# Performance work log

Measured on AMD Instinct MI355X. Metric: run time of the kernel, lower is better.

The kernel has to match this reference:

```python
import jax, jax.numpy as jnp
import numpy as np

FIX_SCALE = np.array([[0.,0.,0.],[1.,0.,0.],[0.,1.,0.],[0.,0.,1.],[-1.,0.,0.],[0.,-1.,0.]], dtype=np.float32)
NUM_HEADS = 8
ATTN_DIMS = 512
HEAD_DIMS = ATTN_DIMS // NUM_HEADS
NUM_LEARN = 6
SIG_CLAMP = 9.21  # safe_sigmoid clamp


def quat_to_rotmat(q):
    # q: [G,4] (w,x,y,z), normalized -> [G,3,3]
    q = q / jnp.linalg.norm(q, axis=-1, keepdims=True)
    w, x, y, z = q[..., 0], q[..., 1], q[..., 2], q[..., 3]
    r0 = jnp.stack([1 - 2*(y*y + z*z), 2*(x*y - w*z), 2*(x*z + w*y)], -1)
    r1 = jnp.stack([2*(x*y + w*z), 1 - 2*(x*x + z*z), 2*(y*z - w*x)], -1)
    r2 = jnp.stack([2*(x*z - w*y), 2*(y*z + w*x), 1 - 2*(x*x + y*y)], -1)
    return jnp.stack([r0, r1, r2], -2)


def bilinear_sample(fm, gx, gy):
    # fm: [C,H,W]; gx,gy: [...] in [-1,1]; align_corners=False, zero padding
    C, H, W = fm.shape
    x = (gx + 1.0) * (W * 0.5) - 0.5
    y = (gy + 1.0) * (H * 0.5) - 0.5
    x0 = jnp.floor(x); y0 = jnp.floor(y)
    wx1 = x - x0; wx0 = 1.0 - wx1
    wy1 = y - y0; wy0 = 1.0 - wy1

    def gather(xf, yf):
        xi = xf.astype(jnp.int32); yi = yf.astype(jnp.int32)
        valid = (xi >= 0) & (xi < W) & (yi >= 0) & (yi < H)
        xi = jnp.clip(xi, 0, W - 1); yi = jnp.clip(yi, 0, H - 1)
        return fm[:, yi, xi] * valid[None].astype(fm.dtype)  # [C, ...]

    out = (gather(x0, y0) * (wx0 * wy0)[None]
           + gather(x0 + 1, y0) * (wx1 * wy0)[None]
           + gather(x0, y0 + 1) * (wx0 * wy1)[None]
           + gather(x0 + 1, y0 + 1) * (wx1 * wy1)[None])
    return jnp.moveaxis(out, 0, -1)  # [..., C]


def setup_inputs() -> dict:
    key = jax.random.key(0)
    ks = jax.random.split(key, 16)
    G, BS, GFD = 8192, 1, 32
    means = jax.random.uniform(ks[0], (G, 3), minval=-1.0, maxval=1.0)
    means = means.at[:, 2].add(3.0)  # push in front of camera
    scales = jax.random.uniform(ks[1], (G, 3), minval=0.01, maxval=0.1)
    rotations = jax.random.normal(ks[2], (G, 4))
    features = jax.random.normal(ks[3], (BS, G, 3, GFD))
    transforms = jnp.tile(jnp.eye(4)[None], (G, 1, 1)) + 0.01 * jax.random.normal(ks[4], (G, 4, 4))
    f = 64.0
    proj = jnp.array([[f, 0., 32., 0.], [0., f, 32., 0.], [0., 0., 1., 0.], [0., 0., 0., 1.]], dtype=jnp.float32)
    projection = jnp.tile(proj[None], (BS, 1, 1))
    image_features = jax.random.normal(ks[5], (BS, 256, 64, 64))
    s = lambda d: 1.0 / np.sqrt(d)
    Wq = jax.random.normal(ks[6], (GFD, ATTN_DIMS)) * s(GFD)
    Wk = jax.random.normal(ks[7], (ATTN_DIMS, 256)) * s(256)
    Wv = jax.random.normal(ks[8], (ATTN_DIMS, 256)) * s(256)
    W_off = jax.random.normal(ks[9], (HEAD_DIMS + 3, NUM_LEARN * 3)) * s(HEAD_DIMS + 3)
    b_off = jnp.zeros((NUM_LEARN * 3,))
    Wout = jax.random.normal(ks[10], (ATTN_DIMS, GFD)) * s(ATTN_DIMS)
    b_out = jnp.zeros((GFD,))
    return {"means": means, "scales": scales, "rotations": rotations, "features": features,
            "transforms": transforms, "projection": projection, "image_features": image_features,
            "Wq": Wq, "Wk": Wk, "Wv": Wv, "W_off": W_off, "b_off": b_off, "Wout": Wout, "b_out": b_out}


def reference(means, scales, rotations, features, transforms, projection, image_features,
              Wq, Wk, Wv, W_off, b_off, Wout, b_out):
    G = means.shape[0]
    bs = features.shape[0]
    H, HD = NUM_HEADS, HEAD_DIMS
    h_img, w_img = image_features.shape[-2:]

    # queries: [bs,G,3,attn] -> [bs,H,G,3,hd]
    q_full = jnp.einsum('bgtf,fa->bgta', features, Wq)
    q = q_full.reshape(bs, G, 3, H, HD).transpose(0, 3, 1, 2, 4)

    # transform means to world space with per-gaussian 4x4
    homo = jnp.concatenate([means, jnp.ones((G, 1), means.dtype)], -1)  # [G,4]
    means_w = jnp.einsum('gij,gj->gi', transforms, homo)[:, :3]  # [G,3]

    # OffsetNet: per-head learnable offsets from (world mean, token-mean query)
    q_mean = q.mean(axis=3)  # [bs,H,G,hd]
    m_b = jnp.broadcast_to(means_w[None, None], (bs, H, G, 3))
    off_in = jnp.concatenate([m_b, q_mean], -1)  # [bs,H,G,hd+3]
    learnable = jax.nn.sigmoid(jnp.clip(off_in @ W_off + b_off, -SIG_CLAMP, SIG_CLAMP))
    learnable = learnable.reshape(bs, H, G, NUM_LEARN, 3) - 0.5
    fix = jnp.broadcast_to(jnp.asarray(FIX_SCALE)[None, None, None], (bs, H, G, FIX_SCALE.shape[0], 3))
    scale_all = jnp.concatenate([fix, learnable], axis=-2)  # [bs,H,G,K,3]
    K = scale_all.shape[-2]

    offset_pts = scale_all * scales[None, None, :, None, :]
    RT = jnp.swapaxes(quat_to_rotmat(rotations), -1, -2)  # [G,3,3]
    offset_pts = jnp.einsum('gij,bhgkj->bhgki', RT, offset_pts) + means_w[None, None, :, None, :]

    # project to 2D, normalize to [0,1), then to grid coords [-1,1]
    pts4 = jnp.concatenate([offset_pts, jnp.ones_like(offset_pts[..., :1])], -1)
    p = jnp.einsum('bij,bhgkj->bhgki', projection, pts4)
    p2 = p[..., :2] / jnp.clip(p[..., 2:3], 1e-5)
    wh = jnp.array([w_img, h_img], dtype=p2.dtype)
    pnorm = jnp.clip(p2 / wh, 0.0, 0.9999)
    grid = 2.0 * pnorm - 1.0  # [bs,H,G,K,2]

    # key/value maps via 1x1 conv, split into per-head channel groups
    kmap = jnp.einsum('ac,bchw->bahw', Wk, image_features).reshape(bs, H, HD, h_img, w_img)
    vmap_ = jnp.einsum('ac,bchw->bahw', Wv, image_features).reshape(bs, H, HD, h_img, w_img)

    sample_bh = jax.vmap(jax.vmap(bilinear_sample, in_axes=(0, 0, 0)), in_axes=(0, 0, 0))
    k_s = sample_bh(kmap, grid[..., 0], grid[..., 1])   # [bs,H,G,K,hd]
    v_s = sample_bh(vmap_, grid[..., 0], grid[..., 1])  # [bs,H,G,K,hd]

    scale = HD ** -0.5
    scores = jnp.einsum('bhgid,bhgkd->bhgik', q, k_s) * scale
    attn = jax.nn.softmax(scores, axis=-1)
    out = jnp.einsum('bhgik,bhgkd->bhgid', attn, v_s)  # [bs,H,G,3,hd]
    out = out.transpose(0, 2, 3, 1, 4).reshape(bs, G, 3, H * HD)  # b g i (h d)
    out = out @ Wout + b_out
    return out + features
```

## Files before the change

### kernel.cpp

```cpp
#include <hip/hip_runtime.h>
#include <hip/hip_bf16.h>
#include <hip/hip_fp16.h>

typedef _Float16 half2v __attribute__((ext_vector_type(2)));
typedef _Float16 half8v __attribute__((ext_vector_type(8)));
typedef __attribute__((ext_vector_type(4))) float float4v;

__device__ __forceinline__ half2v u2h(unsigned u) { return __builtin_bit_cast(half2v, u); }
__device__ __forceinline__ unsigned h2u(half2v h) { return __builtin_bit_cast(unsigned, h); }
__device__ __forceinline__ unsigned short f2hu(float f) {
    _Float16 h = (_Float16)f; return __builtin_bit_cast(unsigned short, h);
}
__device__ __forceinline__ unsigned packh(float lo, float hi) {
    half2v h; h[0] = (_Float16)lo; h[1] = (_Float16)hi; return h2u(h);
}
__device__ __forceinline__ void ld8h(const unsigned short* p, float* f) {
    uint4 u = *(const uint4*)p;
    half2v h0 = u2h(u.x), h1 = u2h(u.y), h2 = u2h(u.z), h3 = u2h(u.w);
    f[0] = (float)h0[0]; f[1] = (float)h0[1]; f[2] = (float)h1[0]; f[3] = (float)h1[1];
    f[4] = (float)h2[0]; f[5] = (float)h2[1]; f[6] = (float)h3[0]; f[7] = (float)h3[1];
}

__global__ __launch_bounds__(256) void offmlp_kernel(
    const float* __restrict__ means, const float* __restrict__ transforms,
    const float* __restrict__ features, const float* __restrict__ Wq,
    const float* __restrict__ W_off, const float* __restrict__ b_off,
    float* __restrict__ lrn_all)
{
    __shared__ __attribute__((aligned(16))) unsigned short Wq16[32 * 512];
    __shared__ float Woffs[1224];
    __shared__ float Wc[36][144];
    __shared__ float A[32][38];
    const int tid = threadIdx.x;
    const int g0 = blockIdx.x * 32;

#pragma unroll
    for (int i = 0; i < 16; i++) {
        int idx4 = i * 256 + tid;
        float4 v = ((const float4*)Wq)[idx4];
        unsigned* dst = (unsigned*)&Wq16[idx4 * 4];
        dst[0] = packh(v.x, v.y);
        dst[1] = packh(v.z, v.w);
    }
    for (int i = tid; i < 1206; i += 256) Woffs[i] = W_off[i];
    if (tid < 18) Woffs[1206 + tid] = b_off[tid];
    {
        const int gi = tid >> 3, sl = tid & 7;
        const int g = g0 + gi;
        const float* fb = features + (size_t)g * 96 + sl * 4;
        float4 t0 = *(const float4*)(fb);
        float4 t1 = *(const float4*)(fb + 32);
        float4 t2 = *(const float4*)(fb + 64);
        A[gi][3 + sl * 4 + 0] = (t0.x + t1.x + t2.x) * (1.f / 3.f);
        A[gi][3 + sl * 4 + 1] = (t0.y + t1.y + t2.y) * (1.f / 3.f);
        A[gi][3 + sl * 4 + 2] = (t0.z + t1.z + t2.z) * (1.f / 3.f);
        A[gi][3 + sl * 4 + 3] = (t0.w + t1.w + t2.w) * (1.f / 3.f);
        if (sl < 3) {
            const float* T = transforms + (size_t)g * 16 + sl * 4;
            float m0 = means[(size_t)g * 3];
            float m1 = means[(size_t)g * 3 + 1];
            float m2 = means[(size_t)g * 3 + 2];
            A[gi][sl] = T[0] * m0 + T[1] * m1 + T[2] * m2 + T[3];
        } else if (sl == 3) {
            A[gi][35] = 1.f;
        }
    }
    __syncthreads();

    for (int k = 0; k < 21; k++) {
        int oi = k * 256 + tid;
        if (oi < 5184) {
            int j = oi / 144, c = oi - j * 144;
            int h = c / 18, l = c - h * 18;
            float v;
            if (j < 3) {
                v = Woffs[j * 18 + l];
            } else if (j == 35) {
                v = Woffs[1206 + l];
            } else {
                int f = j - 3;
                const unsigned* wq2 = (const unsigned*)&Wq16[f * 512 + h * 64];
                float s = 0.f;
#pragma unroll
                for (int d2 = 0; d2 < 32; d2++) {
                    half2v w2 = u2h(wq2[d2]);
                    s += (float)w2[0] * Woffs[(3 + 2 * d2) * 18 + l]
                       + (float)w2[1] * Woffs[(4 + 2 * d2) * 18 + l];
                }
                v = s;
            }
            Wc[j][c] = v;
        }
    }
    __syncthreads();

#pragma unroll
    for (int k = 0; k < 18; k++) {
        int oi = k * 256 + tid;
        int gi = oi / 144, c = oi - gi * 144;
        float s = 0.f;
#pragma unroll
        for (int j = 0; j < 36; j++) s += A[gi][j] * Wc[j][c];
        s = fminf(fmaxf(s, -9.21f), 9.21f);
        lrn_all[(size_t)(g0 + gi) * 144 + c] = 1.f / (1.f + expf(-s)) - 0.5f;
    }
}

__global__ __launch_bounds__(256) void conv_fused_kernel(
    const float* __restrict__ img, const float* __restrict__ Wk,
    const float* __restrict__ Wv, unsigned short* __restrict__ buf)
{
    __shared__ __attribute__((aligned(16))) unsigned short Bt[64][264];
    __shared__ __attribute__((aligned(16))) unsigned short Wt[64][264];
    const int tid = threadIdx.x;
    const int p0 = blockIdx.x * 64;

#pragma unroll
    for (int i = 0; i < 4; i++) {
        int chunk = i * 256 + tid;
        int kp  = chunk >> 3;
        int pxg = (chunk & 7) * 8;
        const float* r0 = img + (size_t)(2 * kp) * 4096 + p0 + pxg;
        const float* r1 = img + (size_t)(2 * kp + 1) * 4096 + p0 + pxg;
        float4 a0 = *(const float4*)r0, a1 = *(const float4*)(r0 + 4);
        float4 b0 = *(const float4*)r1, b1 = *(const float4*)(r1 + 4);
        unsigned lo[8], hi[8];
        lo[0] = f2hu(a0.x); lo[1] = f2hu(a0.y); lo[2] = f2hu(a0.z); lo[3] = f2hu(a0.w);
        lo[4] = f2hu(a1.x); lo[5] = f2hu(a1.y); lo[6] = f2hu(a1.z); lo[7] = f2hu(a1.w);
        hi[0] = f2hu(b0.x); hi[1] = f2hu(b0.y); hi[2] = f2hu(b0.z); hi[3] = f2hu(b0.w);
        hi[4] = f2hu(b1.x); hi[5] = f2hu(b1.y); hi[6] = f2hu(b1.z); hi[7] = f2hu(b1.w);
#pragma unroll
        for (int j = 0; j < 8; j++)
            *(unsigned*)&Bt[pxg + j][2 * kp] = lo[j] | (hi[j] << 16);
    }

    const int w = tid >> 6, l = tid & 63;
    const int m = l & 15, quad = l >> 4;
    const int mrow = w * 16 + m;

#pragma unroll
    for (int j = 0; j < 2; j++) {
        const int o0 = blockIdx.y * 128 + j * 64;
        const float* Wsel = (o0 < 512) ? Wk : Wv;
        const int obase = (o0 < 512) ? o0 : (o0 - 512);
        if (j) __syncthreads();
        {
            const int row = tid >> 2, q = tid & 3;
            const float* wp = Wsel + (size_t)(obase + row) * 256 + q * 64;
#pragma unroll
            for (int jj = 0; jj < 8; jj++) {
                float4 w0 = *(const float4*)(wp + jj * 8);
                float4 w1 = *(const float4*)(wp + jj * 8 + 4);
                uint4 pk;
                pk.x = packh(w0.x, w0.y); pk.y = packh(w0.z, w0.w);
                pk.z = packh(w1.x, w1.y); pk.w = packh(w1.z, w1.w);
                *(uint4*)&Wt[row][q * 64 + jj * 8] = pk;
            }
        }
        __syncthreads();

        float4v acc[4] = {{0,0,0,0},{0,0,0,0},{0,0,0,0},{0,0,0,0}};
#pragma unroll
        for (int kk = 0; kk < 8; kk++) {
            const int kofs = kk * 32 + quad * 8;
            half8v af = *(const half8v*)&Bt[mrow][kofs];
#pragma unroll
            for (int nt = 0; nt < 4; nt++) {
                half8v b8 = *(const half8v*)&Wt[nt * 16 + m][kofs];
                acc[nt] = __builtin_amdgcn_mfma_f32_16x16x32_f16(af, b8, acc[nt], 0, 0, 0);
            }
        }
#pragma unroll
        for (int nt = 0; nt < 4; nt++) {
#pragma unroll
            for (int r = 0; r < 4; r++) {
                size_t px = p0 + w * 16 + quad * 4 + r;
                buf[px * 1024 + o0 + nt * 16 + m] = f2hu(acc[nt][r]);
            }
        }
    }
}

__global__ __launch_bounds__(256) void qgemm_kernel(
    const float* __restrict__ features, const float* __restrict__ Wq,
    unsigned short* __restrict__ qfull)
{
    __shared__ __attribute__((aligned(16))) unsigned short WqT[256][40];
    const int tid = threadIdx.x;
    const int R0 = blockIdx.x * 64;
    const int n0 = blockIdx.y * 256;
#pragma unroll
    for (int k = 0; k < 32; k++)
        WqT[tid][k] = f2hu(Wq[(size_t)k * 512 + n0 + tid]);
    __syncthreads();

    const int w = tid >> 6, l = tid & 63, m = l & 15, quad = l >> 4;
    const int row = R0 + w * 16 + m;
    const float* fp = features + (size_t)row * 32 + quad * 8;
    float4 f0 = *(const float4*)fp, f1 = *(const float4*)(fp + 4);
    half8v af;
    af[0] = (_Float16)f0.x; af[1] = (_Float16)f0.y;
    af[2] = (_Float16)f0.z; af[3] = (_Float16)f0.w;
    af[4] = (_Float16)f1.x; af[5] = (_Float16)f1.y;
    af[6] = (_Float16)f1.z; af[7] = (_Float16)f1.w;
    float4v acc[16];
#pragma unroll
    for (int t = 0; t < 16; t++) acc[t] = (float4v){0.f, 0.f, 0.f, 0.f};
#pragma unroll
    for (int t = 0; t < 16; t++) {
        half8v b8 = *(const half8v*)&WqT[t * 16 + m][quad * 8];
        acc[t] = __builtin_amdgcn_mfma_f32_16x16x32_f16(af, b8, acc[t], 0, 0, 0);
    }
    const int rb = R0 + w * 16 + quad * 4;
#pragma unroll
    for (int t = 0; t < 16; t++)
#pragma unroll
        for (int r = 0; r < 4; r++)
            qfull[(size_t)(rb + r) * 512 + n0 + t * 16 + m] = f2hu(acc[t][r]);
}

__global__ __launch_bounds__(256, 4) void attn_core_kernel(
    const float* __restrict__ means, const float* __restrict__ scales,
    const float* __restrict__ rot,   const float* __restrict__ transforms,
    const float* __restrict__ projection, const float* __restrict__ lrn_all,
    const unsigned short* __restrict__ buf, unsigned short* __restrict__ qfull)
{
    __shared__ __attribute__((aligned(16))) unsigned qf2[768];
    __shared__ __attribute__((aligned(16))) unsigned vsh2[3072];
    __shared__ __attribute__((aligned(16))) uint4 pixwt[96];
    __shared__ __attribute__((aligned(16))) unsigned att2[288];
    __shared__ __attribute__((aligned(16))) float lrnsh[144];
    __shared__ float mw[3], sc3[3], Rt[9], pr[12];

    const int g = blockIdx.x, tid = threadIdx.x;

    if (tid < 36) {
        ((float4*)lrnsh)[tid] = ((const float4*)(lrn_all + (size_t)g * 144))[tid];
    }
    if (tid >= 64 && tid < 67) {
        sc3[tid - 64] = scales[(size_t)g * 3 + (tid - 64)];
    } else if (tid >= 68 && tid < 80) {
// ... 13 lines not shown
        int i = tid - 84;
        float m0 = means[(size_t)g * 3];
        float m1 = means[(size_t)g * 3 + 1];
        float m2 = means[(size_t)g * 3 + 2];
        const float* T = transforms + (size_t)g * 16 + i * 4;
        mw[i] = T[0] * m0 + T[1] * m1 + T[2] * m2 + T[3];
    }
    {
        const unsigned* qsrc = (const unsigned*)(qfull + (size_t)g * 1536);
#pragma unroll
        for (int i = 0; i < 3; i++) qf2[tid + i * 256] = qsrc[tid + i * 256];
    }
    __syncthreads();

    if (tid < 96) {
        int h = tid / 12, k = tid % 12;
        float s0, s1, s2;
        if (k < 6) {
            const float FSx[6] = {0.f, 1.f, 0.f, 0.f, -1.f, 0.f};
            const float FSy[6] = {0.f, 0.f, 1.f, 0.f, 0.f, -1.f};
            const float FSz[6] = {0.f, 0.f, 0.f, 1.f, 0.f, 0.f};
            s0 = FSx[k]; s1 = FSy[k]; s2 = FSz[k];
        } else {
            int b = h * 18 + (k - 6) * 3;
            s0 = lrnsh[b]; s1 = lrnsh[b + 1]; s2 = lrnsh[b + 2];
        }
        float o0 = s0 * sc3[0], o1 = s1 * sc3[1], o2 = s2 * sc3[2];
        float wx = Rt[0] * o0 + Rt[1] * o1 + Rt[2] * o2 + mw[0];
        float wy = Rt[3] * o0 + Rt[4] * o1 + Rt[5] * o2 + mw[1];
        float wz = Rt[6] * o0 + Rt[7] * o1 + Rt[8] * o2 + mw[2];
        float px = pr[0] * wx + pr[1] * wy + pr[2]  * wz + pr[3];
        float py = pr[4] * wx + pr[5] * wy + pr[6]  * wz + pr[7];
        float pz = pr[8] * wx + pr[9] * wy + pr[10] * wz + pr[11];
        pz = fmaxf(pz, 1e-5f);
        float gx = fminf(fmaxf(px / pz * (1.f / 64.f), 0.f), 0.9999f);
        float gy = fminf(fmaxf(py / pz * (1.f / 64.f), 0.f), 0.9999f);
        float x = gx * 64.f - 0.5f, y = gy * 64.f - 0.5f;
        float fx = floorf(x), fy = floorf(y);
        int x0 = (int)fx, y0 = (int)fy;
        float wx1 = x - fx, wy1 = y - fy;
        float wx0 = 1.f - wx1, wy0 = 1.f - wy1;
        int xs[2] = {x0, x0 + 1}, ys[2] = {y0, y0 + 1};
        float wxs[2] = {wx0, wx1}, wys[2] = {wy0, wy1};
        unsigned pix[4]; float wf[4];
#pragma unroll
        for (int c = 0; c < 4; c++) {
            int xi = xs[c & 1], yi = ys[c >> 1];
            bool v = ((unsigned)xi < 64u) & ((unsigned)yi < 64u);
// ... 92 lines not shown
#pragma unroll
        for (int k = 0; k < 12; k++) { float a = e_[k] * inv; rowp[k] = packh(a, a); }
    }
    __syncthreads();

    {
        unsigned* oa32 = (unsigned*)(qfull + (size_t)g * 1536);
#pragma unroll
        for (int i = 0; i < 3; i++) {
            int e = tid + i * 256;
            int t = e >> 8, a2p = e & 255;
            int h = a2p >> 5, ddp = a2p & 31;
            const unsigned* ar2 = att2 + (h * 3 + t) * 12;
            const unsigned* vp  = vsh2 + h * 12 * 32 + ddp;
            half2v acc = {0, 0};
#pragma unroll
            for (int k = 0; k < 12; k++)
                acc += u2h(ar2[k]) * u2h(vp[k * 32]);
            oa32[e] = h2u(acc);
        }
    }
}

__global__ __launch_bounds__(256, 6) void attn_core_basic(
    const float* __restrict__ means, const float* __restrict__ scales,
    const float* __restrict__ rot,   const float* __restrict__ transforms,
    const float* __restrict__ projection, const float* __restrict__ W_off,
    const float* __restrict__ b_off, const unsigned short* __restrict__ buf,
    unsigned short* __restrict__ qfull)
{
    __shared__ __attribute__((aligned(16))) unsigned qf2[768];
    __shared__ __attribute__((aligned(16))) unsigned vsh2[3072];
    __shared__ __attribute__((aligned(16))) float qm_u[512];
    __shared__ __attribute__((aligned(16))) unsigned att2[288];
    __shared__ float mw[3], sc3[3], Rt[9], pr[12];

    float* lrn  = (float*)att2;
    float* wofl = (float*)vsh2;
    float* bofl = wofl + 1206;

    const int g = blockIdx.x, tid = threadIdx.x;

    for (int i = tid; i < 1206; i += 256) wofl[i] = W_off[i];
    if (tid < 18) bofl[tid] = b_off[tid];
    if (tid >= 32 && tid < 35) {
        sc3[tid - 32] = scales[(size_t)g * 3 + (tid - 32)];
// ... 32 lines not shown
    }
    __syncthreads();

    if (tid < 144) {
        int h = tid / 18, l = tid % 18;
        float s = bofl[l];
#pragma unroll
        for (int i = 0; i < 3; i++) s += mw[i] * wofl[i * 18 + l];
        for (int d = 0; d < 64; d++) s += qm_u[h * 64 + d] * wofl[(3 + d) * 18 + l];
        s = fminf(fmaxf(s, -9.21f), 9.21f);
        lrn[tid] = 1.f / (1.f + expf(-s)) - 0.5f;
    }
    __syncthreads();

    if (tid < 96) {
        int h = tid / 12, k = tid % 12;
        float s0, s1, s2;
        if (k < 6) {
            const float FSx[6] = {0.f, 1.f, 0.f, 0.f, -1.f, 0.f};
            const float FSy[6] = {0.f, 0.f, 1.f, 0.f, 0.f, -1.f};
            const float FSz[6] = {0.f, 0.f, 0.f, 1.f, 0.f, 0.f};
            s0 = FSx[k]; s1 = FSy[k]; s2 = FSz[k];
        } else {
            int b = h * 18 + (k - 6) * 3;
            s0 = lrn[b]; s1 = lrn[b + 1]; s2 = lrn[b + 2];
        }
        float o0 = s0 * sc3[0], o1 = s1 * sc3[1], o2 = s2 * sc3[2];
        float wx = Rt[0] * o0 + Rt[1] * o1 + Rt[2] * o2 + mw[0];
        float wy = Rt[3] * o0 + Rt[4] * o1 + Rt[5] * o2 + mw[1];
        float wz = Rt[6] * o0 + Rt[7] * o1 + Rt[8] * o2 + mw[2];
        float px = pr[0] * wx + pr[1] * wy + pr[2]  * wz + pr[3];
        float py = pr[4] * wx + pr[5] * wy + pr[6]  * wz + pr[7];
        float pz = pr[8] * wx + pr[9] * wy + pr[10] * wz + pr[11];
        pz = fmaxf(pz, 1e-5f);
        float gx = fminf(fmaxf(px / pz * (1.f / 64.f), 0.f), 0.9999f);
        float gy = fminf(fmaxf(py / pz * (1.f / 64.f), 0.f), 0.9999f);
        float x = gx * 64.f - 0.5f, y = gy * 64.f - 0.5f;
        float fx = floorf(x), fy = floorf(y);
        int x0 = (int)fx, y0 = (int)fy;
        float wx1 = x - fx, wy1 = y - fy;
        float wx0 = 1.f - wx1, wy0 = 1.f - wy1;
        int xs[2] = {x0, x0 + 1}, ys[2] = {y0, y0 + 1};
        float wxs[2] = {wx0, wx1}, wys[2] = {wy0, wy1};
        unsigned pix[4]; float wf[4];
#pragma unroll
        for (int c = 0; c < 4; c++) {
            int xi = xs[c & 1], yi = ys[c >> 1];
            bool v = ((unsigned)xi < 64u) & ((unsigned)yi < 64u);
// ... 92 lines not shown
#pragma unroll
        for (int k = 0; k < 12; k++) { float a = e_[k] * inv; rowp[k] = packh(a, a); }
    }
    __syncthreads();

    {
        unsigned* oa32 = (unsigned*)(qfull + (size_t)g * 1536);
#pragma unroll
        for (int i = 0; i < 3; i++) {
            int e = tid + i * 256;
            int t = e >> 8, a2p = e & 255;
            int h = a2p >> 5, ddp = a2p & 31;
            const unsigned* ar2 = att2 + (h * 3 + t) * 12;
            const unsigned* vp  = vsh2 + h * 12 * 32 + ddp;
            half2v acc = {0, 0};
#pragma unroll
            for (int k = 0; k < 12; k++)
                acc += u2h(ar2[k]) * u2h(vp[k * 32]);
            oa32[e] = h2u(acc);
        }
    }
}

__global__ __launch_bounds__(256) void outgemm_kernel(
    const unsigned short* __restrict__ oa, const float* __restrict__ Wout,
    const float* __restrict__ b_out, const float* __restrict__ features,
    float* __restrict__ out)
{
    __shared__ __attribute__((aligned(16))) unsigned short WT[32][520];
    const int tid = threadIdx.x;
    const int R0 = blockIdx.x * 64;
#pragma unroll
    for (int j = 0; j < 64; j++) {
        int lin = j * 256 + tid;
        WT[lin & 31][lin >> 5] = f2hu(Wout[lin]);
    }
    __syncthreads();

    const int w = tid >> 6, l = tid & 63, m = l & 15, quad = l >> 4;
    const int row = R0 + w * 16 + m;
    float4v acc[2] = {{0,0,0,0},{0,0,0,0}};
#pragma unroll
    for (int kk = 0; kk < 16; kk++) {
        half8v af = *(const half8v*)(oa + (size_t)row * 512 + kk * 32 + quad * 8);
#pragma unroll
        for (int t = 0; t < 2; t++) {
            half8v b8 = *(const half8v*)&WT[t * 16 + m][kk * 32 + quad * 8];
            acc[t] = __builtin_amdgcn_mfma_f32_16x16x32_f16(af, b8, acc[t], 0, 0, 0);
        }
    }
    const int rb = R0 + w * 16 + quad * 4;
#pragma unroll
    for (int t = 0; t < 2; t++) {
        int col = t * 16 + m;
        float bb = b_out[col];
#pragma unroll
        for (int r = 0; r < 4; r++) {
            int rr = rb + r;
            out[(size_t)rr * 32 + col] = acc[t][r] + bb + features[(size_t)rr * 32 + col];
        }
    }
}

__global__ __launch_bounds__(256, 6) void attn_fused_kernel(
    const float* __restrict__ means, const float* __restrict__ scales,
    const float* __restrict__ rot,   const float* __restrict__ features,
    const float* __restrict__ transforms, const float* __restrict__ projection,
    const float* __restrict__ Wq,    const float* __restrict__ W_off,
    const float* __restrict__ b_off, const float* __restrict__ Wout,
    const float* __restrict__ b_out, const unsigned short* __restrict__ buf,
    float* __restrict__ out)
{
    __shared__ float feat[96];
    __shared__ __attribute__((aligned(16))) float qf[1536];
    __shared__ float qm[512];
    __shared__ float mw[3], sc3[3], Rt[9], pr[12];
    __shared__ float lrn[144];
    __shared__ int   coff[96][4];
    __shared__ float cwt[96][4];
    __shared__ __attribute__((aligned(16))) char pool[12288];
    __shared__ float att[288];

    unsigned short* vsh = (unsigned short*)pool;
    const int g = blockIdx.x, tid = threadIdx.x;

    if (tid < 96) {
// ... 44 lines not shown
    qm[tid + 256] = (qf[tid + 256] + qf[tid + 768] + qf[tid + 1280]) * (1.f / 3.f);
    __syncthreads();

    if (tid < 144) {
        int h = tid / 18, l = tid % 18;
        float s = b_off[l];
#pragma unroll
        for (int i = 0; i < 3; i++) s += mw[i] * W_off[i * 18 + l];
        for (int d = 0; d < 64; d++) s += qm[h * 64 + d] * W_off[(size_t)(3 + d) * 18 + l];
        s = fminf(fmaxf(s, -9.21f), 9.21f);
        lrn[tid] = 1.f / (1.f + expf(-s)) - 0.5f;
    }
    __syncthreads();

    if (tid < 96) {
        int h = tid / 12, k = tid % 12;
        float s0, s1, s2;
        if (k < 6) {
            const float FSx[6] = {0.f, 1.f, 0.f, 0.f, -1.f, 0.f};
            const float FSy[6] = {0.f, 0.f, 1.f, 0.f, 0.f, -1.f};
            const float FSz[6] = {0.f, 0.f, 0.f, 1.f, 0.f, 0.f};
            s0 = FSx[k]; s1 = FSy[k]; s2 = FSz[k];
        } else {
            int b = h * 18 + (k - 6) * 3;
            s0 = lrn[b]; s1 = lrn[b + 1]; s2 = lrn[b + 2];
        }
        float o0 = s0 * sc3[0], o1 = s1 * sc3[1], o2 = s2 * sc3[2];
        float wx = Rt[0] * o0 + Rt[1] * o1 + Rt[2] * o2 + mw[0];
        float wy = Rt[3] * o0 + Rt[4] * o1 + Rt[5] * o2 + mw[1];
        float wz = Rt[6] * o0 + Rt[7] * o1 + Rt[8] * o2 + mw[2];
        float px = pr[0] * wx + pr[1] * wy + pr[2]  * wz + pr[3];
        float py = pr[4] * wx + pr[5] * wy + pr[6]  * wz + pr[7];
        float pz = pr[8] * wx + pr[9] * wy + pr[10] * wz + pr[11];
        pz = fmaxf(pz, 1e-5f);
        float gx = fminf(fmaxf(px / pz * (1.f / 64.f), 0.f), 0.9999f);
        float gy = fminf(fmaxf(py / pz * (1.f / 64.f), 0.f), 0.9999f);
        float x = gx * 64.f - 0.5f, y = gy * 64.f - 0.5f;
        float fx = floorf(x), fy = floorf(y);
        int x0 = (int)fx, y0 = (int)fy;
        float wx1 = x - fx, wx0c = 1.f - wx1;
        float wy1 = y - fy, wy0c = 1.f - wy1;
        int xs[2] = {x0, x0 + 1}, ys[2] = {y0, y0 + 1};
        float wxs[2] = {wx0c, wx1}, wys[2] = {wy0c, wy1};
#pragma unroll
        for (int c = 0; c < 4; c++) {
            int dx = c & 1, dy = c >> 1;
            int xi = xs[dx], yi = ys[dy];
            bool v = (xi >= 0) & (xi < 64) & (yi >= 0) & (yi < 64);
// ... 116 lines not shown
    const float* scales     = (const float*)d_in[1];
    const float* rot        = (const float*)d_in[2];
    const float* features   = (const float*)d_in[3];
    const float* transforms = (const float*)d_in[4];
    const float* projection = (const float*)d_in[5];
    const float* img        = (const float*)d_in[6];
    const float* Wq         = (const float*)d_in[7];
    const float* Wk         = (const float*)d_in[8];
    const float* Wv         = (const float*)d_in[9];
    const float* W_off      = (const float*)d_in[10];
    const float* b_off      = (const float*)d_in[11];
    const float* Wout       = (const float*)d_in[12];
    const float* b_out      = (const float*)d_in[13];
    float* out = (float*)d_out;

    char* w = (char*)d_ws;
    unsigned short* buf = (unsigned short*)(w + 64);
    const size_t BUF_BYTES = (size_t)4096 * 1024 * 2;
    const size_t Q_BYTES   = (size_t)24576 * 512 * 2;
    const size_t LRN_BYTES = (size_t)8192 * 144 * 4;
    const size_t need  = 64 + BUF_BYTES + Q_BYTES;
    const size_t need2 = need + LRN_BYTES;

    dim3 gridc(64, 8);
    conv_fused_kernel<<<gridc, 256, 0, stream>>>(img, Wk, Wv, buf);

    if (ws_size >= need2) {
        unsigned short* qfull = (unsigned short*)(w + 64 + BUF_BYTES);
        float* lrn_all = (float*)(w + 64 + BUF_BYTES + Q_BYTES);

        offmlp_kernel<<<256, 256, 0, stream>>>(
            means, transforms, features, Wq, W_off, b_off, lrn_all);
        dim3 gridq(384, 2);
        qgemm_kernel<<<gridq, 256, 0, stream>>>(features, Wq, qfull);
        attn_core_kernel<<<8192, 256, 0, stream>>>(
            means, scales, rot, transforms, projection, lrn_all, buf, qfull);
        outgemm_kernel<<<384, 256, 0, stream>>>(qfull, Wout, b_out, features, out);
    } else if (ws_size >= need) {
        unsigned short* qfull = (unsigned short*)(w + 64 + BUF_BYTES);
        dim3 gridq(384, 2);
        qgemm_kernel<<<gridq, 256, 0, stream>>>(features, Wq, qfull);
        attn_core_basic<<<8192, 256, 0, stream>>>(
            means, scales, rot, transforms, projection, W_off, b_off, buf, qfull);
        outgemm_kernel<<<384, 256, 0, stream>>>(qfull, Wout, b_out, features, out);
    } else {
        attn_fused_kernel<<<8192, 256, 0, stream>>>(
            means, scales, rot, features, transforms, projection,
            Wq, W_off, b_off, Wout, b_out, buf, out);
    }
}
```

Measured before the change: 182.0 us.

## Merge conv, offset-MLP and Q-GEMM prologue kernels into one launch

Replaces three separate launches (1x1 conv K/V projection, offset MLP, Q projection) with a single mega kernel whose blocks branch on blockIdx to run each independent job over shared LDS pooled storage. The conv part now uses one 64-channel tile per block (1024 blocks) instead of looping over two tiles, and the offset-MLP blocks each handle 128 gaussians so the fused weight matrix is built fewer times. The goal is to remove launch gaps and tail underutilisation between small kernels. The cost is that LDS is sized for the largest branch, which may reduce occupancy for the lighter branches.

```diff
diff --git a/kernel.cpp b/kernel.cpp
--- a/kernel.cpp
+++ b/kernel.cpp
@@ -21,143 +21,62 @@
     f[4] = (float)h2[0]; f[5] = (float)h2[1]; f[6] = (float)h3[0]; f[7] = (float)h3[1];
 }
 
-__global__ __launch_bounds__(256) void offmlp_kernel(
-    const float* __restrict__ means, const float* __restrict__ transforms,
-    const float* __restrict__ features, const float* __restrict__ Wq,
-    const float* __restrict__ W_off, const float* __restrict__ b_off,
-    float* __restrict__ lrn_all)
+__global__ __launch_bounds__(256) void mega_kernel(
+    const float* __restrict__ img, const float* __restrict__ Wk,
+    const float* __restrict__ Wv, const float* __restrict__ features,
+    const float* __restrict__ Wq, const float* __restrict__ means,
+    const float* __restrict__ transforms, const float* __restrict__ W_off,
+    const float* __restrict__ b_off, unsigned short* __restrict__ buf,
+    unsigned short* __restrict__ qfull, float* __restrict__ lrn_all)
 {
-    __shared__ __attribute__((aligned(16))) unsigned short Wq16[32 * 512];
-    __shared__ float Woffs[1224];
-    __shared__ float Wc[36][144];
-    __shared__ float A[32][38];
+    __shared__ __attribute__((aligned(16))) unsigned short POOL[2 * 64 * 264];
     const int tid = threadIdx.x;
-    const int g0 = blockIdx.x * 32;
-
-#pragma unroll
-    for (int i = 0; i < 16; i++) {
-        int idx4 = i * 256 + tid;
-        float4 v = ((const float4*)Wq)[idx4];
-        unsigned* dst = (unsigned*)&Wq16[idx4 * 4];
-        dst[0] = packh(v.x, v.y);
-        dst[1] = packh(v.z, v.w);
-    }
-    for (int i = tid; i < 1206; i += 256) Woffs[i] = W_off[i];
-    if (tid < 18) Woffs[1206 + tid] = b_off[tid];
-    {
-        const int gi = tid >> 3, sl = tid & 7;
-        const int g = g0 + gi;
-        const float* fb = features + (size_t)g * 96 + sl * 4;
-        float4 t0 = *(const float4*)(fb);
-        float4 t1 = *(const float4*)(fb + 32);
-        float4 t2 = *(const float4*)(fb + 64);
-        A[gi][3 + sl * 4 + 0] = (t0.x + t1.x + t2.x) * (1.f / 3.f);
-        A[gi][3 + sl * 4 + 1] = (t0.y + t1.y + t2.y) * (1.f / 3.f);
-        A[gi][3 + sl * 4 + 2] = (t0.z + t1.z + t2.z) * (1.f / 3.f);
-        A[gi][3 + sl * 4 + 3] = (t0.w + t1.w + t2.w) * (1.f / 3.f);
-        if (sl < 3) {
-            const float* T = transforms + (size_t)g * 16 + sl * 4;
-            float m0 = means[(size_t)g * 3];
-            float m1 = means[(size_t)g * 3 + 1];
-            float m2 = means[(size_t)g * 3 + 2];
-            A[gi][sl] = T[0] * m0 + T[1] * m1 + T[2] * m2 + T[3];
-        } else if (sl == 3) {
-            A[gi][35] = 1.f;
-        }
-    }
-    __syncthreads();
-
-    for (int k = 0; k < 21; k++) {
-        int oi = k * 256 + tid;
-        if (oi < 5184) {
-            int j = oi / 144, c = oi - j * 144;
-            int h = c / 18, l = c - h * 18;
-            float v;
-            if (j < 3) {
-                v = Woffs[j * 18 + l];
-            } else if (j == 35) {
-                v = Woffs[1206 + l];
-            } else {
-                int f = j - 3;
-                const unsigned* wq2 = (const unsigned*)&Wq16[f * 512 + h * 64];
-                float s = 0.f;
-#pragma unroll
-                for (int d2 = 0; d2 < 32; d2++) {
-                    half2v w2 = u2h(wq2[d2]);
-                    s += (float)w2[0] * Woffs[(3 + 2 * d2) * 18 + l]
-                       + (float)w2[1] * Woffs[(4 + 2 * d2) * 18 + l];
-                }
-                v = s;
-            }
-            Wc[j][c] = v;
-        }
-    }
-    __syncthreads();
-
-#pragma unroll
-    for (int k = 0; k < 18; k++) {
-        int oi = k * 256 + tid;
-        int gi = oi / 144, c = oi - gi * 144;
-        float s = 0.f;
-#pragma unroll
-        for (int j = 0; j < 36; j++) s += A[gi][j] * Wc[j][c];
-        s = fminf(fmaxf(s, -9.21f), 9.21f);
-        lrn_all[(size_t)(g0 + gi) * 144 + c] = 1.f / (1.f + expf(-s)) - 0.5f;
-    }
-}
-
-__global__ __launch_bounds__(256) void conv_fused_kernel(
-    const float* __restrict__ img, const float* __restrict__ Wk,
-    const float* __restrict__ Wv, unsigned short* __restrict__ buf)
-{
-    __shared__ __attribute__((aligned(16))) unsigned short Bt[64][264];
-    __shared__ __attribute__((aligned(16))) unsigned short Wt[64][264];
-    const int tid = threadIdx.x;
-    const int p0 = blockIdx.x * 64;
-
-#pragma unroll
-    for (int i = 0; i < 4; i++) {
-        int chunk = i * 256 + tid;
-        int kp  = chunk >> 3;
-        int pxg = (chunk & 7) * 8;
-        const float* r0 = img + (size_t)(2 * kp) * 4096 + p0 + pxg;
-        const float* r1 = img + (size_t)(2 * kp + 1) * 4096 + p0 + pxg;
-        float4 a0 = *(const float4*)r0, a1 = *(const float4*)(r0 + 4);
-        float4 b0 = *(const float4*)r1, b1 = *(const float4*)(r1 + 4);
-        unsigned lo[8], hi[8];
-        lo[0] = f2hu(a0.x); lo[1] = f2hu(a0.y); lo[2] = f2hu(a0.z); lo[3] = f2hu(a0.w);
-        lo[4] = f2hu(a1.x); lo[5] = f2hu(a1.y); lo[6] = f2hu(a1.z); lo[7] = f2hu(a1.w);
-        hi[0] = f2hu(b0.x); hi[1] = f2hu(b0.y); hi[2] = f2hu(b0.z); hi[3] = f2hu(b0.w);
-        hi[4] = f2hu(b1.x); hi[5] = f2hu(b1.y); hi[6] = f2hu(b1.z); hi[7] = f2hu(b1.w);
-#pragma unroll
-        for (int j = 0; j < 8; j++)
-            *(unsigned*)&Bt[pxg + j][2 * kp] = lo[j] | (hi[j] << 16);
-    }
-
-    const int w = tid >> 6, l = tid & 63;
-    const int m = l & 15, quad = l >> 4;
-    const int mrow = w * 16 + m;
-
-#pragma unroll
-    for (int j = 0; j < 2; j++) {
-        const int o0 = blockIdx.y * 128 + j * 64;
+    const int b = blockIdx.x;
+
+    if (b < 1024) {
+        unsigned short (*Bt)[264] = (unsigned short (*)[264])POOL;
+        unsigned short (*Wt)[264] = (unsigned short (*)[264])(POOL + 64 * 264);
+        const int p0 = (b & 63) * 64;
+        const int o0 = (b >> 6) * 64;
         const float* Wsel = (o0 < 512) ? Wk : Wv;
         const int obase = (o0 < 512) ? o0 : (o0 - 512);
-        if (j) __syncthreads();
+
+#pragma unroll
+        for (int i = 0; i < 4; i++) {
+            int chunk = i * 256 + tid;
+            int kp  = chunk >> 3;
+            int pxg = (chunk & 7) * 8;
+            const float* r0 = img + (size_t)(2 * kp) * 4096 + p0 + pxg;
+            const float* r1 = img + (size_t)(2 * kp + 1) * 4096 + p0 + pxg;
+            float4 a0 = *(const float4*)r0, a1 = *(const float4*)(r0 + 4);
+            float4 b0 = *(const float4*)r1, b1 = *(const float4*)(r1 + 4);
+            unsigned lo[8], hi[8];
+            lo[0] = f2hu(a0.x); lo[1] = f2hu(a0.y); lo[2] = f2hu(a0.z); lo[3] = f2hu(a0.w);
+            lo[4] = f2hu(a1.x); lo[5] = f2hu(a1.y); lo[6] = f2hu(a1.z); lo[7] = f2hu(a1.w);
+            hi[0] = f2hu(b0.x); hi[1] = f2hu(b0.y); hi[2] = f2hu(b0.z); hi[3] = f2hu(b0.w);
+            hi[4] = f2hu(b1.x); hi[5] = f2hu(b1.y); hi[6] = f2hu(b1.z); hi[7] = f2hu(b1.w);
+#pragma unroll
+            for (int j = 0; j < 8; j++)
+                *(unsigned*)&Bt[pxg + j][2 * kp] = lo[j] | (hi[j] << 16);
+        }
         {
             const int row = tid >> 2, q = tid & 3;
             const float* wp = Wsel + (size_t)(obase + row) * 256 + q * 64;
 #pragma unroll
-            for (int jj = 0; jj < 8; jj++) {
-                float4 w0 = *(const float4*)(wp + jj * 8);
-                float4 w1 = *(const float4*)(wp + jj * 8 + 4);
+            for (int j = 0; j < 8; j++) {
+                float4 w0 = *(const float4*)(wp + j * 8);
+                float4 w1 = *(const float4*)(wp + j * 8 + 4);
                 uint4 pk;
                 pk.x = packh(w0.x, w0.y); pk.y = packh(w0.z, w0.w);
                 pk.z = packh(w1.x, w1.y); pk.w = packh(w1.z, w1.w);
-                *(uint4*)&Wt[row][q * 64 + jj * 8] = pk;
+                *(uint4*)&Wt[row][q * 64 + j * 8] = pk;
             }
         }
         __syncthreads();
+
+        const int w = tid >> 6, l = tid & 63;
+        const int m = l & 15, quad = l >> 4;
+        const int mrow = w * 16 + m;
 
         float4v acc[4] = {{0,0,0,0},{0,0,0,0},{0,0,0,0},{0,0,0,0}};
 #pragma unroll
@@ -178,45 +97,122 @@
                 buf[px * 1024 + o0 + nt * 16 + m] = f2hu(acc[nt][r]);
             }
         }
-    }
-}
-
-__global__ __launch_bounds__(256) void qgemm_kernel(
-    const float* __restrict__ features, const float* __restrict__ Wq,
-    unsigned short* __restrict__ qfull)
-{
-    __shared__ __attribute__((aligned(16))) unsigned short WqT[256][40];
-    const int tid = threadIdx.x;
-    const int R0 = blockIdx.x * 64;
-    const int n0 = blockIdx.y * 256;
-#pragma unroll
-    for (int k = 0; k < 32; k++)
-        WqT[tid][k] = f2hu(Wq[(size_t)k * 512 + n0 + tid]);
-    __syncthreads();
-
-    const int w = tid >> 6, l = tid & 63, m = l & 15, quad = l >> 4;
-    const int row = R0 + w * 16 + m;
-    const float* fp = features + (size_t)row * 32 + quad * 8;
-    float4 f0 = *(const float4*)fp, f1 = *(const float4*)(fp + 4);
-    half8v af;
-    af[0] = (_Float16)f0.x; af[1] = (_Float16)f0.y;
-    af[2] = (_Float16)f0.z; af[3] = (_Float16)f0.w;
-    af[4] = (_Float16)f1.x; af[5] = (_Float16)f1.y;
-    af[6] = (_Float16)f1.z; af[7] = (_Float16)f1.w;
-    float4v acc[16];
-#pragma unroll
-    for (int t = 0; t < 16; t++) acc[t] = (float4v){0.f, 0.f, 0.f, 0.f};
-#pragma unroll
-    for (int t = 0; t < 16; t++) {
-        half8v b8 = *(const half8v*)&WqT[t * 16 + m][quad * 8];
-        acc[t] = __builtin_amdgcn_mfma_f32_16x16x32_f16(af, b8, acc[t], 0, 0, 0);
-    }
-    const int rb = R0 + w * 16 + quad * 4;
-#pragma unroll
-    for (int t = 0; t < 16; t++)
-#pragma unroll
-        for (int r = 0; r < 4; r++)
-            qfull[(size_t)(rb + r) * 512 + n0 + t * 16 + m] = f2hu(acc[t][r]);
+    } else if (b < 1088) {
+        unsigned short* Wq16 = POOL;
+        float* Woffs = (float*)((char*)POOL + 32768);
+        float (*Wc)[144] = (float (*)[144])((char*)POOL + 37664);
+        float (*A)[38]   = (float (*)[38])((char*)POOL + 58400);
+        const int blk = b - 1024;
+
+#pragma unroll
+        for (int i = 0; i < 16; i++) {
+            int idx4 = i * 256 + tid;
+            float4 v = ((const float4*)Wq)[idx4];
+            unsigned* dst = (unsigned*)&Wq16[idx4 * 4];
+            dst[0] = packh(v.x, v.y);
+            dst[1] = packh(v.z, v.w);
+        }
+        for (int i = tid; i < 1206; i += 256) Woffs[i] = W_off[i];
+        if (tid < 18) Woffs[1206 + tid] = b_off[tid];
+        __syncthreads();
+
+        for (int k = 0; k < 21; k++) {
+            int oi = k * 256 + tid;
+            if (oi < 5184) {
+                int j = oi / 144, c = oi - j * 144;
+                int h = c / 18, l = c - h * 18;
+                float v;
+                if (j < 3) {
+                    v = Woffs[j * 18 + l];
+                } else if (j == 35) {
+                    v = Woffs[1206 + l];
+                } else {
+                    int f = j - 3;
+                    const unsigned* wq2 = (const unsigned*)&Wq16[f * 512 + h * 64];
+                    float s = 0.f;
+#pragma unroll
+                    for (int d2 = 0; d2 < 32; d2++) {
+                        half2v w2 = u2h(wq2[d2]);
+                        s += (float)w2[0] * Woffs[(3 + 2 * d2) * 18 + l]
+                           + (float)w2[1] * Woffs[(4 + 2 * d2) * 18 + l];
+                    }
+                    v = s;
+                }
+                Wc[j][c] = v;
+            }
+        }
+        __syncthreads();
+
+        for (int ch = 0; ch < 4; ch++) {
+            const int g0 = blk * 128 + ch * 32;
+            {
+                const int gi = tid >> 3, sl = tid & 7;
+                const int g = g0 + gi;
+                const float* fb = features + (size_t)g * 96 + sl * 4;
+                float4 t0 = *(const float4*)(fb);
+                float4 t1 = *(const float4*)(fb + 32);
+                float4 t2 = *(const float4*)(fb + 64);
+                A[gi][3 + sl * 4 + 0] = (t0.x + t1.x + t2.x) * (1.f / 3.f);
+                A[gi][3 + sl * 4 + 1] = (t0.y + t1.y + t2.y) * (1.f / 3.f);
+                A[gi][3 + sl * 4 + 2] = (t0.z + t1.z + t2.z) * (1.f / 3.f);
+                A[gi][3 + sl * 4 + 3] = (t0.w + t1.w + t2.w) * (1.f / 3.f);
+                if (sl < 3) {
+                    const float* T = transforms + (size_t)g * 16 + sl * 4;
+                    float m0 = means[(size_t)g * 3];
+                    float m1 = means[(size_t)g * 3 + 1];
+                    float m2 = means[(size_t)g * 3 + 2];
+                    A[gi][sl] = T[0] * m0 + T[1] * m1 + T[2] * m2 + T[3];
+                } else if (sl == 3) {
+                    A[gi][35] = 1.f;
+                }
+            }
+            __syncthreads();
+#pragma unroll
+            for (int k = 0; k < 18; k++) {
+                int oi = k * 256 + tid;
+                int gi = oi / 144, c = oi - gi * 144;
+                float s = 0.f;
+#pragma unroll
+                for (int j = 0; j < 36; j++) s += A[gi][j] * Wc[j][c];
+                s = fminf(fmaxf(s, -9.21f), 9.21f);
+                lrn_all[(size_t)(g0 + gi) * 144 + c] = 1.f / (1.f + expf(-s)) - 0.5f;
+            }
+            __syncthreads();
+        }
+    } else {
+        unsigned short (*WqT)[40] = (unsigned short (*)[40])POOL;
+        const int qb = b - 1088;
+        const int R0 = (qb >> 1) * 64;
+        const int n0 = (qb & 1) * 256;
+#pragma unroll
+        for (int k = 0; k < 32; k++)
+            WqT[tid][k] = f2hu(Wq[(size_t)k * 512 + n0 + tid]);
+        __syncthreads();
+
+        const int w = tid >> 6, l = tid & 63, m = l & 15, quad = l >> 4;
+        const int row = R0 + w * 16 + m;
+        const float* fp = features + (size_t)row * 32 + quad * 8;
+        float4 f0 = *(const float4*)fp, f1 = *(const float4*)(fp + 4);
+        half8v af;
+        af[0] = (_Float16)f0.x; af[1] = (_Float16)f0.y;
+        af[2] = (_Float16)f0.z; af[3] = (_Float16)f0.w;
+        af[4] = (_Float16)f1.x; af[5] = (_Float16)f1.y;
+        af[6] = (_Float16)f1.z; af[7] = (_Float16)f1.w;
+        float4v acc[16];
+#pragma unroll
+        for (int t = 0; t < 16; t++) acc[t] = (float4v){0.f, 0.f, 0.f, 0.f};
+#pragma unroll
+        for (int t = 0; t < 16; t++) {
+            half8v b8 = *(const half8v*)&WqT[t * 16 + m][quad * 8];
+            acc[t] = __builtin_amdgcn_mfma_f32_16x16x32_f16(af, b8, acc[t], 0, 0, 0);
+        }
+        const int rb = R0 + w * 16 + quad * 4;
+#pragma unroll
+        for (int t = 0; t < 16; t++)
+#pragma unroll
+            for (int r = 0; r < 4; r++)
+                qfull[(size_t)(rb + r) * 512 + n0 + t * 16 + m] = f2hu(acc[t][r]);
+    }
 }
 
 __global__ __launch_bounds__(256, 4) void attn_core_kernel(
@@ -276,8 +272,8 @@
             const float FSz[6] = {0.f, 0.f, 0.f, 1.f, 0.f, 0.f};
             s0 = FSx[k]; s1 = FSy[k]; s2 = FSz[k];
         } else {
-            int b = h * 18 + (k - 6) * 3;
-            s0 = lrnsh[b]; s1 = lrnsh[b + 1]; s2 = lrnsh[b + 2];
+            int bq = h * 18 + (k - 6) * 3;
+            s0 = lrnsh[bq]; s1 = lrnsh[bq + 1]; s2 = lrnsh[bq + 2];
         }
         float o0 = s0 * sc3[0], o1 = s1 * sc3[1], o2 = s2 * sc3[2];
         float wx = Rt[0] * o0 + Rt[1] * o1 + Rt[2] * o2 + mw[0];
@@ -416,6 +412,154 @@
     }
 }
 
+__global__ __launch_bounds__(256) void outgemm_kernel(
+    const unsigned short* __restrict__ oa, const float* __restrict__ Wout,
+    const float* __restrict__ b_out, const float* __restrict__ features,
+    float* __restrict__ out)
+{
+    __shared__ __attribute__((aligned(16))) unsigned short WT[32][520];
+    const int tid = threadIdx.x;
+    const int R0 = blockIdx.x * 64;
+#pragma unroll
+    for (int j = 0; j < 64; j++) {
+        int lin = j * 256 + tid;
+        WT[lin & 31][lin >> 5] = f2hu(Wout[lin]);
+    }
+    __syncthreads();
+
+    const int w = tid >> 6, l = tid & 63, m = l & 15, quad = l >> 4;
+    const int row = R0 + w * 16 + m;
+    float4v acc[2] = {{0,0,0,0},{0,0,0,0}};
+#pragma unroll
+    for (int kk = 0; kk < 16; kk++) {
+        half8v af = *(const half8v*)(oa + (size_t)row * 512 + kk * 32 + quad * 8);
+#pragma unroll
+        for (int t = 0; t < 2; t++) {
+            half8v b8 = *(const half8v*)&WT[t * 16 + m][kk * 32 + quad * 8];
+            acc[t] = __builtin_amdgcn_mfma_f32_16x16x32_f16(af, b8, acc[t], 0, 0, 0);
+        }
+    }
+    const int rb = R0 + w * 16 + quad * 4;
+#pragma unroll
+    for (int t = 0; t < 2; t++) {
+        int col = t * 16 + m;
+        float bb = b_out[col];
+#pragma unroll
+        for (int r = 0; r < 4; r++) {
+            int rr = rb + r;
+            out[(size_t)rr * 32 + col] = acc[t][r] + bb + features[(size_t)rr * 32 + col];
+        }
+    }
+}
+
+__global__ __launch_bounds__(256) void conv_fused_kernel(
+    const float* __restrict__ img, const float* __restrict__ Wk,
+    const float* __restrict__ Wv, unsigned short* __restrict__ buf)
+{
+    __shared__ __attribute__((aligned(16))) unsigned short Bt[64][264];
+    __shared__ __attribute__((aligned(16))) unsigned short Wt[64][264];
+    const int tid = threadIdx.x;
+    const int p0 = blockIdx.x * 64;
+    const int o0 = blockIdx.y * 64;
+    const float* Wsel = (o0 < 512) ? Wk : Wv;
+    const int obase = (o0 < 512) ? o0 : (o0 - 512);
+
+#pragma unroll
+    for (int i = 0; i < 4; i++) {
+        int chunk = i * 256 + tid;
+        int kp  = chunk >> 3;
+        int pxg = (chunk & 7) * 8;
+        const float* r0 = img + (size_t)(2 * kp) * 4096 + p0 + pxg;
+        const float* r1 = img + (size_t)(2 * kp + 1) * 4096 + p0 + pxg;
+        float4 a0 = *(const float4*)r0, a1 = *(const float4*)(r0 + 4);
+        float4 b0 = *(const float4*)r1, b1 = *(const float4*)(r1 + 4);
+        unsigned lo[8], hi[8];
+        lo[0] = f2hu(a0.x); lo[1] = f2hu(a0.y); lo[2] = f2hu(a0.z); lo[3] = f2hu(a0.w);
+        lo[4] = f2hu(a1.x); lo[5] = f2hu(a1.y); lo[6] = f2hu(a1.z); lo[7] = f2hu(a1.w);
+        hi[0] = f2hu(b0.x); hi[1] = f2hu(b0.y); hi[2] = f2hu(b0.z); hi[3] = f2hu(b0.w);
+        hi[4] = f2hu(b1.x); hi[5] = f2hu(b1.y); hi[6] = f2hu(b1.z); hi[7] = f2hu(b1.w);
+#pragma unroll
+        for (int j = 0; j < 8; j++)
+            *(unsigned*)&Bt[pxg + j][2 * kp] = lo[j] | (hi[j] << 16);
+    }
+    {
+        const int row = tid >> 2, q = tid & 3;
+        const float* wp = Wsel + (size_t)(obase + row) * 256 + q * 64;
+#pragma unroll
+        for (int j = 0; j < 8; j++) {
+            float4 w0 = *(const float4*)(wp + j * 8);
+            float4 w1 = *(const float4*)(wp + j * 8 + 4);
+            uint4 pk;
+            pk.x = packh(w0.x, w0.y); pk.y = packh(w0.z, w0.w);
+            pk.z = packh(w1.x, w1.y); pk.w = packh(w1.z, w1.w);
+            *(uint4*)&Wt[row][q * 64 + j * 8] = pk;
+        }
+    }
+    __syncthreads();
+
+    const int w = tid >> 6, l = tid & 63;
+    const int m = l & 15, quad = l >> 4;
+    const int mrow = w * 16 + m;
+
+    float4v acc[4] = {{0,0,0,0},{0,0,0,0},{0,0,0,0},{0,0,0,0}};
+#pragma unroll
+    for (int kk = 0; kk < 8; kk++) {
+        const int kofs = kk * 32 + quad * 8;
+        half8v af = *(const half8v*)&Bt[mrow][kofs];
+#pragma unroll
+        for (int nt = 0; nt < 4; nt++) {
+            half8v b8 = *(const half8v*)&Wt[nt * 16 + m][kofs];
+            acc[nt] = __builtin_amdgcn_mfma_f32_16x16x32_f16(af, b8, acc[nt], 0, 0, 0);
+        }
+    }
+#pragma unroll
+    for (int nt = 0; nt < 4; nt++) {
+#pragma unroll
+        for (int r = 0; r < 4; r++) {
+            size_t px = p0 + w * 16 + quad * 4 + r;
+            buf[px * 1024 + o0 + nt * 16 + m] = f2hu(acc[nt][r]);
+        }
+    }
+}
+
+__global__ __launch_bounds__(256) void qgemm_kernel(
+    const float* __restrict__ features, const float* __restrict__ Wq,
+    unsigned short* __restrict__ qfull)
+{
+    __shared__ __attribute__((aligned(16))) unsigned short WqT[256][40];
+    const int tid = threadIdx.x;
+    const int R0 = blockIdx.x * 64;
+    const int n0 = blockIdx.y * 256;
+#pragma unroll
+    for (int k = 0; k < 32; k++)
+        WqT[tid][k] = f2hu(Wq[(size_t)k * 512 + n0 + tid]);
+    __syncthreads();
+
+    const int w = tid >> 6, l = tid & 63, m = l & 15, quad = l >> 4;
+    const int row = R0 + w * 16 + m;
+    const float* fp = features + (size_t)row * 32 + quad * 8;
+    float4 f0 = *(const float4*)fp, f1 = *(const float4*)(fp + 4);
+    half8v af;
+    af[0] = (_Float16)f0.x; af[1] = (_Float16)f0.y;
+    af[2] = (_Float16)f0.z; af[3] = (_Float16)f0.w;
+    af[4] = (_Float16)f1.x; af[5] = (_Float16)f1.y;
+    af[6] = (_Float16)f1.z; af[7] = (_Float16)f1.w;
+    float4v acc[16];
+#pragma unroll
+    for (int t = 0; t < 16; t++) acc[t] = (float4v){0.f, 0.f, 0.f, 0.f};
+#pragma unroll
+    for (int t = 0; t < 16; t++) {
+        half8v b8 = *(const half8v*)&WqT[t * 16 + m][quad * 8];
+        acc[t] = __builtin_amdgcn_mfma_f32_16x16x32_f16(af, b8, acc[t], 0, 0, 0);
+    }
+    const int rb = R0 + w * 16 + quad * 4;
+#pragma unroll
+    for (int t = 0; t < 16; t++)
+#pragma unroll
+        for (int r = 0; r < 4; r++)
+            qfull[(size_t)(rb + r) * 512 + n0 + t * 16 + m] = f2hu(acc[t][r]);
+}
+
 __global__ __launch_bounds__(256, 6) void attn_core_basic(
     const float* __restrict__ means, const float* __restrict__ scales,
     const float* __restrict__ rot,   const float* __restrict__ transforms,
@@ -494,8 +638,8 @@
             const float FSz[6] = {0.f, 0.f, 0.f, 1.f, 0.f, 0.f};
             s0 = FSx[k]; s1 = FSy[k]; s2 = FSz[k];
         } else {
-            int b = h * 18 + (k - 6) * 3;
-            s0 = lrn[b]; s1 = lrn[b + 1]; s2 = lrn[b + 2];
+            int bq = h * 18 + (k - 6) * 3;
+            s0 = lrn[bq]; s1 = lrn[bq + 1]; s2 = lrn[bq + 2];
         }
         float o0 = s0 * sc3[0], o1 = s1 * sc3[1], o2 = s2 * sc3[2];
         float wx = Rt[0] * o0 + Rt[1] * o1 + Rt[2] * o2 + mw[0];
@@ -634,46 +778,6 @@
     }
 }
 
-__global__ __launch_bounds__(256) void outgemm_kernel(
-    const unsigned short* __restrict__ oa, const float* __restrict__ Wout,
-    const float* __restrict__ b_out, const float* __restrict__ features,
-    float* __restrict__ out)
-{
-    __shared__ __attribute__((aligned(16))) unsigned short WT[32][520];
-    const int tid = threadIdx.x;
-    const int R0 = blockIdx.x * 64;
-#pragma unroll
-    for (int j = 0; j < 64; j++) {
-        int lin = j * 256 + tid;
-        WT[lin & 31][lin >> 5] = f2hu(Wout[lin]);
-    }
-    __syncthreads();
-
-    const int w = tid >> 6, l = tid & 63, m = l & 15, quad = l >> 4;
-    const int row = R0 + w * 16 + m;
-    float4v acc[2] = {{0,0,0,0},{0,0,0,0}};
-#pragma unroll
-    for (int kk = 0; kk < 16; kk++) {
-        half8v af = *(const half8v*)(oa + (size_t)row * 512 + kk * 32 + quad * 8);
-#pragma unroll
-        for (int t = 0; t < 2; t++) {
-            half8v b8 = *(const half8v*)&WT[t * 16 + m][kk * 32 + quad * 8];
-            acc[t] = __builtin_amdgcn_mfma_f32_16x16x32_f16(af, b8, acc[t], 0, 0, 0);
-        }
-    }
-    const int rb = R0 + w * 16 + quad * 4;
-#pragma unroll
-    for (int t = 0; t < 2; t++) {
-        int col = t * 16 + m;
-        float bb = b_out[col];
-#pragma unroll
-        for (int r = 0; r < 4; r++) {
-            int rr = rb + r;
-            out[(size_t)rr * 32 + col] = acc[t][r] + bb + features[(size_t)rr * 32 + col];
-        }
-    }
-}
-
 __global__ __launch_bounds__(256, 6) void attn_fused_kernel(
     const float* __restrict__ means, const float* __restrict__ scales,
     const float* __restrict__ rot,   const float* __restrict__ features,
@@ -764,8 +868,8 @@
             const float FSz[6] = {0.f, 0.f, 0.f, 1.f, 0.f, 0.f};
             s0 = FSx[k]; s1 = FSy[k]; s2 = FSz[k];
         } else {
-            int b = h * 18 + (k - 6) * 3;
-            s0 = lrn[b]; s1 = lrn[b + 1]; s2 = lrn[b + 2];
+            int bq = h * 18 + (k - 6) * 3;
+            s0 = lrn[bq]; s1 = lrn[bq + 1]; s2 = lrn[bq + 2];
         }
         float o0 = s0 * sc3[0], o1 = s1 * sc3[1], o2 = s2 * sc3[2];
         float wx = Rt[0] * o0 + Rt[1] * o1 + Rt[2] * o2 + mw[0];
@@ -928,28 +1032,28 @@
     const size_t need  = 64 + BUF_BYTES + Q_BYTES;
     const size_t need2 = need + LRN_BYTES;
 
-    dim3 gridc(64, 8);
-    conv_fused_kernel<<<gridc, 256, 0, stream>>>(img, Wk, Wv, buf);
-
     if (ws_size >= need2) {
         unsigned short* qfull = (unsigned short*)(w + 64 + BUF_BYTES);
         float* lrn_all = (float*)(w + 64 + BUF_BYTES + Q_BYTES);
 
-        offmlp_kernel<<<256, 256, 0, stream>>>(
-            means, transforms, features, Wq, W_off, b_off, lrn_all);
-        dim3 gridq(384, 2);
-        qgemm_kernel<<<gridq, 256, 0, stream>>>(features, Wq, qfull);
+        mega_kernel<<<1856, 256, 0, stream>>>(
+            img, Wk, Wv, features, Wq, means, transforms, W_off, b_off,
+            buf, qfull, lrn_all);
         attn_core_kernel<<<8192, 256, 0, stream>>>(
             means, scales, rot, transforms, projection, lrn_all, buf, qfull);
         outgemm_kernel<<<384, 256, 0, stream>>>(qfull, Wout, b_out, features, out);
     } else if (ws_size >= need) {
         unsigned short* qfull = (unsigned short*)(w + 64 + BUF_BYTES);
+        dim3 gridc(64, 16);
+        conv_fused_kernel<<<gridc, 256, 0, stream>>>(img, Wk, Wv, buf);
         dim3 gridq(384, 2);
         qgemm_kernel<<<gridq, 256, 0, stream>>>(features, Wq, qfull);
         attn_core_basic<<<8192, 256, 0, stream>>>(
             means, scales, rot, transforms, projection, W_off, b_off, buf, qfull);
         outgemm_kernel<<<384, 256, 0, stream>>>(qfull, Wout, b_out, features, out);
     } else {
+        dim3 gridc(64, 16);
+        conv_fused_kernel<<<gridc, 256, 0, stream>>>(img, Wk, Wv, buf);
         attn_fused_kernel<<<8192, 256, 0, stream>>>(
             means, scales, rot, features, transforms, projection,
             Wq, W_off, b_off, Wout, b_out, buf, out);
```

Result: slower. 220.8 us (+21.3%).
